# Kernel tuning notes

Measured on AMD Instinct MI355X. Metric: run time of the kernel, lower is better.

## Reference

```python
import jax, jax.numpy as jnp
import numpy as np

NUM_HEADS = 16
D_MODEL = 1024
D_KV = 64
NUM_BUCKETS = 32
MAX_DISTANCE = 128


def _relative_position_bucket(relative_position, num_buckets=NUM_BUCKETS, max_distance=MAX_DISTANCE):
    # faithful port of the torch static method (bidirectional variant)
    n = -relative_position
    nb = num_buckets // 2
    ret = (n < 0).astype(jnp.int32) * nb
    n = jnp.abs(n)
    max_exact = nb // 2
    is_small = n < max_exact
    # guard log(0); is_small branch covers n < max_exact anyway
    val_if_large = max_exact + (
        jnp.log(jnp.maximum(n, 1).astype(jnp.float32) / max_exact)
        / np.log(max_distance / max_exact)
        * (nb - max_exact)
    ).astype(jnp.int32)
    val_if_large = jnp.minimum(val_if_large, nb - 1)
    return ret + jnp.where(is_small, n, val_if_large)


def _compute_bias(seq_len, rel_bias):
    ctx = jnp.arange(seq_len)[:, None]
    mem = jnp.arange(seq_len)[None, :]
    bucket = _relative_position_bucket(mem - ctx)  # [S, S]
    values = rel_bias[bucket]                      # [S, S, H]
    return jnp.transpose(values, (2, 0, 1))[None]  # [1, H, S, S]


def setup_inputs() -> dict:
    key = jax.random.key(0)
    ks = jax.random.split(key, 6)
    B, S = 4, 1024
    scale = 1.0 / np.sqrt(D_MODEL)
    return {
        "hidden_states": jax.random.normal(ks[0], (B, S, D_MODEL), jnp.float32),
        "attention_mask": jnp.ones((B, 1, 1, S), jnp.int32),
        "Wq": jax.random.normal(ks[1], (NUM_HEADS * D_KV, D_MODEL), jnp.float32) * scale,
        "Wk": jax.random.normal(ks[2], (NUM_HEADS * D_KV, D_MODEL), jnp.float32) * scale,
        "Wv": jax.random.normal(ks[3], (NUM_HEADS * D_KV, D_MODEL), jnp.float32) * scale,
        "Wo": jax.random.normal(ks[4], (D_MODEL, NUM_HEADS * D_KV), jnp.float32) * scale,
        "rel_bias": jax.random.normal(ks[5], (NUM_BUCKETS, NUM_HEADS), jnp.float32),
    }


def reference(hidden_states, attention_mask, Wq, Wk, Wv, Wo, rel_bias):
    B, S, _ = hidden_states.shape
    # projections (Linear with bias=False: x @ W.T), reshape to [B, S, H, d_kv]
    q = jnp.einsum('bsd,ed->bse', hidden_states, Wq).reshape(B, S, NUM_HEADS, D_KV)
    k = jnp.einsum('bsd,ed->bse', hidden_states, Wk).reshape(B, S, NUM_HEADS, D_KV)
    v = jnp.einsum('bsd,ed->bse', hidden_states, Wv).reshape(B, S, NUM_HEADS, D_KV)
    scores = jnp.einsum('bqhd,bkhd->bhqk', q, k) / np.sqrt(D_KV)
    scores = scores + _compute_bias(S, rel_bias)
    scores = jnp.where(attention_mask == 0, jnp.float32(-1e9), scores)
    attn_weights = jax.nn.softmax(scores, axis=-1)  # dropout is identity at eval
    attn_output = jnp.einsum('bhqk,bkhd->bqhd', attn_weights, v).reshape(B, S, NUM_HEADS * D_KV)
    output = jnp.einsum('bse,de->bsd', attn_output, Wo)
    return output, attn_weights
```

## Files before the change

### kernel.cpp

```cpp
#include <hip/hip_runtime.h>
#include <hip/hip_bf16.h>

#define BB 4
#define SS 1024
#define HH 16
#define DK 64
#define DM 1024
#define MM (BB * SS)

typedef __attribute__((ext_vector_type(8))) short bh8_t;
typedef __attribute__((ext_vector_type(4))) float f4_t;

#define MFMA(a, b, c) __builtin_amdgcn_mfma_f32_16x16x32_bf16(a, b, c, 0, 0, 0)

__device__ __forceinline__ short f2bf(float f) {
    unsigned u = __builtin_bit_cast(unsigned, f);
    u = (u + 0x7FFFu + ((u >> 16) & 1u)) >> 16;
    return (short)u;
}
__device__ __forceinline__ float bf2f(short h) {
    unsigned u = ((unsigned)(unsigned short)h) << 16;
    return __builtin_bit_cast(float, u);
}

__device__ __forceinline__ int rel_bucket(int rel) {
    int n = -rel;
    int ret = 0;
    if (n < 0) { ret = 16; n = -n; }
    int v;
    if (n < 8) {
        v = n;
    } else {
        float t = logf((float)n * 0.125f) / 2.7725887298583984f * 8.0f;
        v = 8 + (int)t;
        if (v > 15) v = 15;
    }
    return ret + v;
}

__global__ __launch_bounds__(256)
void k_proj(const float* __restrict__ X, const float* __restrict__ Wq,
            const float* __restrict__ Wk, const float* __restrict__ Wv,
            short* __restrict__ Qh, short* __restrict__ Ql,
            short* __restrict__ Kh, short* __restrict__ Kl,
            short* __restrict__ Vt) {
    const int z = blockIdx.z;

    __shared__ short Ah[128][40], Al[128][40], Bh[128][40], Bl[128][40];

    const int tid = threadIdx.x;
    const int m0 = blockIdx.y * 128, n0 = blockIdx.x * 128;
    const int wave = tid >> 6, lane = tid & 63;
    const int quad = lane >> 4, lm = lane & 15;
    const int wm = (wave >> 1) * 64, wn = (wave & 1) * 64;
    const int r = tid >> 1, sg = (tid & 1) * 16;

    f4_t acc[4][4];
#pragma unroll
    for (int i = 0; i < 4; ++i)
#pragma unroll
        for (int j = 0; j < 4; ++j) acc[i][j] = (f4_t){0.f, 0.f, 0.f, 0.f};

    if (z < 2) {
        const float* W = z ? Wk : Wq;
        short* Oh = z ? Kh : Qh;
        short* Ol = z ? Kl : Ql;

        for (int k0 = 0; k0 < DM; k0 += 32) {
            f4_t xa[4], wb[4];
#pragma unroll
            for (int u = 0; u < 4; ++u) {
                xa[u] = *(const f4_t*)(X + (size_t)(m0 + r) * DM + k0 + sg + u * 4);
                wb[u] = *(const f4_t*)(W + (size_t)(n0 + r) * DM + k0 + sg + u * 4);
            }
            __syncthreads();
#pragma unroll
            for (int u = 0; u < 4; ++u) {
                short4 hh, ll;
                hh.x = f2bf(xa[u][0]); ll.x = f2bf(xa[u][0] - bf2f(hh.x));
                hh.y = f2bf(xa[u][1]); ll.y = f2bf(xa[u][1] - bf2f(hh.y));
                hh.z = f2bf(xa[u][2]); ll.z = f2bf(xa[u][2] - bf2f(hh.z));
                hh.w = f2bf(xa[u][3]); ll.w = f2bf(xa[u][3] - bf2f(hh.w));
                *(short4*)&Ah[r][sg + u * 4] = hh;
                *(short4*)&Al[r][sg + u * 4] = ll;
                hh.x = f2bf(wb[u][0]); ll.x = f2bf(wb[u][0] - bf2f(hh.x));
                hh.y = f2bf(wb[u][1]); ll.y = f2bf(wb[u][1] - bf2f(hh.y));
                hh.z = f2bf(wb[u][2]); ll.z = f2bf(wb[u][2] - bf2f(hh.z));
                hh.w = f2bf(wb[u][3]); ll.w = f2bf(wb[u][3] - bf2f(hh.w));
                *(short4*)&Bh[r][sg + u * 4] = hh;
                *(short4*)&Bl[r][sg + u * 4] = ll;
            }
            __syncthreads();

            bh8_t ah[4], al[4];
#pragma unroll
            for (int i = 0; i < 4; ++i) {
                ah[i] = *(const bh8_t*)&Ah[wm + i * 16 + lm][quad * 8];
                al[i] = *(const bh8_t*)&Al[wm + i * 16 + lm][quad * 8];
            }
#pragma unroll
            for (int j = 0; j < 4; ++j) {
                bh8_t bhj = *(const bh8_t*)&Bh[wn + j * 16 + lm][quad * 8];
                bh8_t blj = *(const bh8_t*)&Bl[wn + j * 16 + lm][quad * 8];
#pragma unroll
                for (int i = 0; i < 4; ++i) {
                    acc[i][j] = MFMA(al[i], bhj, acc[i][j]);
                    acc[i][j] = MFMA(ah[i], blj, acc[i][j]);
                    acc[i][j] = MFMA(ah[i], bhj, acc[i][j]);
                }
            }
        }

#pragma unroll
        for (int i = 0; i < 4; ++i)
#pragma unroll
            for (int j = 0; j < 4; ++j)
#pragma unroll
                for (int g = 0; g < 4; ++g) {
                    const int row = m0 + wm + i * 16 + quad * 4 + g;
                    const int col = n0 + wn + j * 16 + lm;
                    const int b = row >> 10, s = row & 1023;
                    const int hd = col >> 6, dk = col & 63;
                    const float v = acc[i][j][g];
                    const short vh = f2bf(v);
                    const short vl = f2bf(v - bf2f(vh));
                    const size_t o = ((size_t)((b * HH + hd) * SS + s)) * DK + dk;
                    Oh[o] = vh;
                    Ol[o] = vl;
                }
    } else {
        for (int k0 = 0; k0 < DM; k0 += 32) {
            f4_t xa[4], wb[4];
#pragma unroll
            for (int u = 0; u < 4; ++u) {
                xa[u] = *(const f4_t*)(X + (size_t)(m0 + r) * DM + k0 + sg + u * 4);
                wb[u] = *(const f4_t*)(Wv + (size_t)(n0 + r) * DM + k0 + sg + u * 4);
            }
            __syncthreads();
#pragma unroll
            for (int u = 0; u < 4; ++u) {
                short4 hh;
                hh.x = f2bf(xa[u][0]); hh.y = f2bf(xa[u][1]);
                hh.z = f2bf(xa[u][2]); hh.w = f2bf(xa[u][3]);
                *(short4*)&Ah[r][sg + u * 4] = hh;
                hh.x = f2bf(wb[u][0]); hh.y = f2bf(wb[u][1]);
                hh.z = f2bf(wb[u][2]); hh.w = f2bf(wb[u][3]);
                *(short4*)&Bh[r][sg + u * 4] = hh;
            }
            __syncthreads();

            bh8_t ah[4];
#pragma unroll
            for (int i = 0; i < 4; ++i)
                ah[i] = *(const bh8_t*)&Ah[wm + i * 16 + lm][quad * 8];
#pragma unroll
            for (int j = 0; j < 4; ++j) {
                bh8_t bhj = *(const bh8_t*)&Bh[wn + j * 16 + lm][quad * 8];
#pragma unroll
                for (int i = 0; i < 4; ++i) acc[i][j] = MFMA(ah[i], bhj, acc[i][j]);
            }
        }

#pragma unroll
        for (int i = 0; i < 4; ++i)
#pragma unroll
            for (int j = 0; j < 4; ++j)
#pragma unroll
                for (int g = 0; g < 4; ++g) {
                    const int row = m0 + wm + i * 16 + quad * 4 + g;
                    const int col = n0 + wn + j * 16 + lm;
                    const int b = row >> 10, s = row & 1023;
                    const int hd = col >> 6, dk = col & 63;
                    Vt[((size_t)((b * HH + hd) * DK + dk)) * SS + s] = f2bf(acc[i][j][g]);
                }
    }
}

#define EPAD 1044

__global__ __launch_bounds__(512, 4)
void k_fused(const short* __restrict__ Qh, const short* __restrict__ Ql,
             const short* __restrict__ Kh, const short* __restrict__ Kl,
             const short* __restrict__ Vt, const int* __restrict__ mask,
             const float* __restrict__ rb, float* __restrict__ P,
             short* __restrict__ AO) {
    __shared__ __align__(16) char smem[75584];
    float* E     = (float*)smem;
    float* redS  = (float*)smem;
    float* biasS = (float*)(smem + 66816);
    int*   maskS = (int*)(smem + 70976);
    float* wmaxS = (float*)(smem + 75072);

    const int tid = threadIdx.x;
    const int bid = blockIdx.x;
    const int swz = (bid & 7) * 512 + (bid >> 3);
    const int qb = swz & 63, bh = swz >> 6;
    const int b = bh >> 4, hd = bh & 15;
    const int q0 = qb * 16;
    const int wave = tid >> 6, lane = tid & 63;
    const int quad = lane >> 4, lm = lane & 15;

    for (int i = tid; i < 1040; i += 512)
        biasS[i] = rb[rel_bucket(i - q0 - 15) * HH + hd];
    for (int i = tid; i < 1024; i += 512) maskS[i] = mask[b * SS + i];

    bh8_t qah[2], qal[2];
#pragma unroll
    for (int ks = 0; ks < 2; ++ks) {
        const size_t qo = ((size_t)bh * SS + q0 + lm) * DK + ks * 32 + quad * 8;
        qah[ks] = *(const bh8_t*)(Qh + qo);
        qal[ks] = *(const bh8_t*)(Ql + qo);
    }
    __syncthreads();

    float pmax[4] = {-3.0e38f, -3.0e38f, -3.0e38f, -3.0e38f};

#pragma unroll
    for (int kt = 0; kt < 4; ++kt) {
        const int kb = wave * 128 + kt * 32;
        f4_t acc[2];
        acc[0] = (f4_t){0.f, 0.f, 0.f, 0.f};
        acc[1] = (f4_t){0.f, 0.f, 0.f, 0.f};
        bh8_t kh[2][2], kl[2][2];
#pragma unroll
        for (int j = 0; j < 2; ++j)
#pragma unroll
            for (int ks = 0; ks < 2; ++ks) {
                const size_t ko =
                    ((size_t)bh * SS + kb + j * 16 + lm) * DK + ks * 32 + quad * 8;
                kh[j][ks] = *(const bh8_t*)(Kh + ko);
                kl[j][ks] = *(const bh8_t*)(Kl + ko);
            }
#pragma unroll
        for (int j = 0; j < 2; ++j)
#pragma unroll
            for (int ks = 0; ks < 2; ++ks) {
                acc[j] = MFMA(qal[ks], kh[j][ks], acc[j]);
                acc[j] = MFMA(qah[ks], kl[j][ks], acc[j]);
                acc[j] = MFMA(qah[ks], kh[j][ks], acc[j]);
            }
#pragma unroll
        for (int j = 0; j < 2; ++j) {
            const int col = kb + j * 16 + lm;
            const int msk = maskS[col];
#pragma unroll
            for (int g = 0; g < 4; ++g) {
                const int rl = quad * 4 + g;
                float s = acc[j][g] * 0.125f + biasS[col - rl + 15];
                s = (msk == 0) ? -1e9f : s;
                E[rl * EPAD + col] = s;
                pmax[g] = fmaxf(pmax[g], s);
            }
        }
    }
#pragma unroll
    for (int g = 0; g < 4; ++g) {
        float m = pmax[g];
        m = fmaxf(m, __shfl_xor(m, 1, 64));
        m = fmaxf(m, __shfl_xor(m, 2, 64));
        m = fmaxf(m, __shfl_xor(m, 4, 64));
        m = fmaxf(m, __shfl_xor(m, 8, 64));
        if (lm == 0) wmaxS[wave * 16 + quad * 4 + g] = m;
    }
    __syncthreads();

    {
        const int row = tid >> 5;
        const int cc = (tid & 31) * 4;
        float m = wmaxS[row];
#pragma unroll
        for (int w = 1; w < 8; ++w) m = fmaxf(m, wmaxS[w * 16 + row]);
        f4_t ev[8];
        float sum = 0.f;
#pragma unroll
        for (int u = 0; u < 8; ++u) {
            f4_t s4 = *(const f4_t*)&E[row * EPAD + cc + u * 128];
            f4_t e;
            e[0] = __expf(s4[0] - m);
            e[1] = __expf(s4[1] - m);
            e[2] = __expf(s4[2] - m);
            e[3] = __expf(s4[3] - m);
            ev[u] = e;
            sum += e[0] + e[1] + e[2] + e[3];
        }
        sum += __shfl_xor(sum, 1, 64);
        sum += __shfl_xor(sum, 2, 64);
        sum += __shfl_xor(sum, 4, 64);
        sum += __shfl_xor(sum, 8, 64);
        sum += __shfl_xor(sum, 16, 64);
        const float inv = 1.0f / sum;
        float* Pr = P + ((size_t)bh * SS + q0 + row) * SS;
#pragma unroll
        for (int u = 0; u < 8; ++u) {
            f4_t p;
            p[0] = ev[u][0] * inv;
            p[1] = ev[u][1] * inv;
            p[2] = ev[u][2] * inv;
            p[3] = ev[u][3] * inv;
            *(f4_t*)&E[row * EPAD + cc + u * 128] = p;
            *(f4_t*)(Pr + cc + u * 128) = p;
        }
    }
    __syncthreads();

    f4_t acc[4];
#pragma unroll
    for (int f = 0; f < 4; ++f) acc[f] = (f4_t){0.f, 0.f, 0.f, 0.f};

#pragma unroll
    for (int kk = 0; kk < 4; ++kk) {
        const int kg = wave * 128 + kk * 32 + quad * 8;
        f4_t p0 = *(const f4_t*)&E[lm * EPAD + kg];
        f4_t p1 = *(const f4_t*)&E[lm * EPAD + kg + 4];
        bh8_t pa;
        pa[0] = f2bf(p0[0]); pa[1] = f2bf(p0[1]);
        pa[2] = f2bf(p0[2]); pa[3] = f2bf(p0[3]);
        pa[4] = f2bf(p1[0]); pa[5] = f2bf(p1[1]);
        pa[6] = f2bf(p1[2]); pa[7] = f2bf(p1[3]);
#pragma unroll
        for (int f = 0; f < 4; ++f) {
            bh8_t vb =
                *(const bh8_t*)(Vt + ((size_t)bh * DK + f * 16 + lm) * SS + kg);
            acc[f] = MFMA(pa, vb, acc[f]);
        }
    }
    __syncthreads();
#pragma unroll
    for (int f = 0; f < 4; ++f)
#pragma unroll
        for (int g = 0; g < 4; ++g)
            redS[((size_t)wave * 16 + quad * 4 + g) * 64 + f * 16 + lm] = acc[f][g];
    __syncthreads();

    {
        const int flat = tid * 2;
        const int q = flat >> 6, dk = flat & 63;
        float s0 = 0.f, s1 = 0.f;
#pragma unroll
        for (int w = 0; w < 8; ++w) {
            s0 += redS[((size_t)w * 16 + q) * 64 + dk];
            s1 += redS[((size_t)w * 16 + q) * 64 + dk + 1];
        }
        short2 o;
        o.x = f2bf(s0);
        o.y = f2bf(s1);
        *(short2*)(AO + ((size_t)(b * SS + q0 + q)) * DM + hd * DK + dk) = o;
    }
}

__global__ __launch_bounds__(256)
void k_out(const short* __restrict__ A, const float* __restrict__ Wo,
           float* __restrict__ Out) {
    __shared__ short As[128][40], Bs[128][40];

    const int tid = threadIdx.x;
    const int m0 = blockIdx.y * 128, n0 = blockIdx.x * 128;
    const int wave = tid >> 6, lane = tid & 63;
    const int quad = lane >> 4, lm = lane & 15;
    const int wm = (wave >> 1) * 64, wn = (wave & 1) * 64;
    const int r = tid >> 1, sg = (tid & 1) * 16;

    f4_t acc[4][4];
#pragma unroll
    for (int i = 0; i < 4; ++i)
#pragma unroll
        for (int j = 0; j < 4; ++j) acc[i][j] = (f4_t){0.f, 0.f, 0.f, 0.f};

    for (int k0 = 0; k0 < DM; k0 += 32) {
        uint4 a0 = *(const uint4*)(A + (size_t)(m0 + r) * DM + k0 + sg);
        uint4 a1 = *(const uint4*)(A + (size_t)(m0 + r) * DM + k0 + sg + 8);
        f4_t wb[4];
#pragma unroll
        for (int u = 0; u < 4; ++u)
            wb[u] = *(const f4_t*)(Wo + (size_t)(n0 + r) * DM + k0 + sg + u * 4);
        __syncthreads();
        *(uint4*)&As[r][sg] = a0;
        *(uint4*)&As[r][sg + 8] = a1;
#pragma unroll
        for (int u = 0; u < 4; ++u) {
            short4 hh;
            hh.x = f2bf(wb[u][0]); hh.y = f2bf(wb[u][1]);
            hh.z = f2bf(wb[u][2]); hh.w = f2bf(wb[u][3]);
            *(short4*)&Bs[r][sg + u * 4] = hh;
        }
        __syncthreads();

        bh8_t ah[4];
#pragma unroll
        for (int i = 0; i < 4; ++i)
            ah[i] = *(const bh8_t*)&As[wm + i * 16 + lm][quad * 8];
#pragma unroll
        for (int j = 0; j < 4; ++j) {
            bh8_t bhj = *(const bh8_t*)&Bs[wn + j * 16 + lm][quad * 8];
#pragma unroll
            for (int i = 0; i < 4; ++i) acc[i][j] = MFMA(ah[i], bhj, acc[i][j]);
        }
    }

#pragma unroll
    for (int i = 0; i < 4; ++i)
#pragma unroll
        for (int j = 0; j < 4; ++j)
#pragma unroll
            for (int g = 0; g < 4; ++g)
                Out[(size_t)(m0 + wm + i * 16 + quad * 4 + g) * DM + n0 + wn + j * 16 + lm] =
                    acc[i][j][g];
}

extern "C" void kernel_launch(void* const* d_in, const int* in_sizes, int n_in,
                              void* d_out, int out_size, void* d_ws, size_t ws_size,
                              hipStream_t stream) {
    const float* X    = (const float*)d_in[0];
    const int*   mask = (const int*)d_in[1];
    const float* Wq   = (const float*)d_in[2];
    const float* Wk   = (const float*)d_in[3];
    const float* Wv   = (const float*)d_in[4];
    const float* Wo   = (const float*)d_in[5];
    const float* rb   = (const float*)d_in[6];

    float* out = (float*)d_out;
    float* P   = out + (size_t)BB * SS * DM;

    short* ws = (short*)d_ws;
    short* Qh = ws;
    short* Ql = ws + (size_t)4194304;
    short* Kh = ws + (size_t)8388608;
    short* Kl = ws + (size_t)12582912;
    short* Vt = ws + (size_t)16777216;
    short* AO = ws + (size_t)20971520;

    k_proj <<<dim3(8, 32, 3), 256, 0, stream>>>(X, Wq, Wk, Wv, Qh, Ql, Kh, Kl, Vt);
    k_fused<<<dim3(4096), 512, 0, stream>>>(Qh, Ql, Kh, Kl, Vt, mask, rb, P, AO);
    k_out  <<<dim3(8, 32), 256, 0, stream>>>(AO, Wo, out);
}
```

Baseline: 645.5 us.

## Pre-split inputs to bf16 hi/lo, precompute bias table, prefetch tiles, stream P stores

Adds a k_split pre-pass that converts X and the weights to bf16 hi/lo pairs once and builds a per-head relative-bias table. This replaces the repeated fp32 loads and conversions inside every GEMM tile and the log-based bucket computation per block. The GEMMs and the attention kernel now register-prefetch the next K/V/A/B tile while computing the current one. The attention-probability write moves after the PV product, reading E with coalesced rows and using nontemporal stores, and some syncthreads become raw s_barrier. In exchange it adds an extra launch and extra workspace traffic for the split copies.

```diff
diff --git a/kernel.cpp b/kernel.cpp
--- a/kernel.cpp
+++ b/kernel.cpp
@@ -39,8 +39,50 @@
 }
 
 __global__ __launch_bounds__(256)
-void k_proj(const float* __restrict__ X, const float* __restrict__ Wq,
-            const float* __restrict__ Wk, const float* __restrict__ Wv,
+void k_split(const float* __restrict__ X, const float* __restrict__ Wq,
+             const float* __restrict__ Wk, const float* __restrict__ Wv,
+             const float* __restrict__ Wo, const float* __restrict__ rbv,
+             short* __restrict__ Xh, short* __restrict__ Xl,
+             short* __restrict__ Wqh, short* __restrict__ Wql,
+             short* __restrict__ Wkh, short* __restrict__ Wkl,
+             short* __restrict__ Wvh, short* __restrict__ Woh,
+             float* __restrict__ biasT) {
+    const long i = (long)blockIdx.x * 256 + threadIdx.x;
+    if (i < 2097152) {
+        const float* src;
+        short* dh;
+        short* dl = nullptr;
+        long j = i;
+        if (i < 1048576) { src = X; dh = Xh; dl = Xl; }
+        else if (i < 1310720) { src = Wq; dh = Wqh; dl = Wql; j = i - 1048576; }
+        else if (i < 1572864) { src = Wk; dh = Wkh; dl = Wkl; j = i - 1310720; }
+        else if (i < 1835008) { src = Wv; dh = Wvh; j = i - 1572864; }
+        else { src = Wo; dh = Woh; j = i - 1835008; }
+        f4_t v = *(const f4_t*)(src + j * 4);
+        short4 h, l;
+        h.x = f2bf(v[0]); l.x = f2bf(v[0] - bf2f(h.x));
+        h.y = f2bf(v[1]); l.y = f2bf(v[1] - bf2f(h.y));
+        h.z = f2bf(v[2]); l.z = f2bf(v[2] - bf2f(h.z));
+        h.w = f2bf(v[3]); l.w = f2bf(v[3] - bf2f(h.w));
+        *(short4*)(dh + j * 4) = h;
+        if (dl) *(short4*)(dl + j * 4) = l;
+    } else if (i < 2105408) {
+        const long j = i - 2097152;
+        const int hd = (int)(j / 516);
+        const int d0 = (int)(j % 516) * 4;
+#pragma unroll
+        for (int t = 0; t < 4; ++t) {
+            const int dd = d0 + t;
+            biasT[hd * 2064 + dd] = rbv[rel_bucket(dd - 1024) * HH + hd];
+        }
+    }
+}
+
+__global__ __launch_bounds__(256)
+void k_proj(const short* __restrict__ Xh, const short* __restrict__ Xl,
+            const short* __restrict__ Wqh, const short* __restrict__ Wql,
+            const short* __restrict__ Wkh, const short* __restrict__ Wkl,
+            const short* __restrict__ Wvh,
             short* __restrict__ Qh, short* __restrict__ Ql,
             short* __restrict__ Kh, short* __restrict__ Kl,
             short* __restrict__ Vt) {
@@ -61,36 +103,34 @@
 #pragma unroll
         for (int j = 0; j < 4; ++j) acc[i][j] = (f4_t){0.f, 0.f, 0.f, 0.f};
 
+    const size_t xoff = (size_t)(m0 + r) * DM + sg;
+    const size_t woff = (size_t)(n0 + r) * DM + sg;
+
     if (z < 2) {
-        const float* W = z ? Wk : Wq;
+        const short* Wh = z ? Wkh : Wqh;
+        const short* Wl = z ? Wkl : Wql;
         short* Oh = z ? Kh : Qh;
         short* Ol = z ? Kl : Ql;
 
+        uint4 a0 = *(const uint4*)(Xh + xoff), a1 = *(const uint4*)(Xh + xoff + 8);
+        uint4 c0 = *(const uint4*)(Xl + xoff), c1 = *(const uint4*)(Xl + xoff + 8);
+        uint4 b0 = *(const uint4*)(Wh + woff), b1 = *(const uint4*)(Wh + woff + 8);
+        uint4 d0 = *(const uint4*)(Wl + woff), d1 = *(const uint4*)(Wl + woff + 8);
+
         for (int k0 = 0; k0 < DM; k0 += 32) {
-            f4_t xa[4], wb[4];
-#pragma unroll
-            for (int u = 0; u < 4; ++u) {
-                xa[u] = *(const f4_t*)(X + (size_t)(m0 + r) * DM + k0 + sg + u * 4);
-                wb[u] = *(const f4_t*)(W + (size_t)(n0 + r) * DM + k0 + sg + u * 4);
-            }
             __syncthreads();
-#pragma unroll
-            for (int u = 0; u < 4; ++u) {
-                short4 hh, ll;
-                hh.x = f2bf(xa[u][0]); ll.x = f2bf(xa[u][0] - bf2f(hh.x));
-                hh.y = f2bf(xa[u][1]); ll.y = f2bf(xa[u][1] - bf2f(hh.y));
-                hh.z = f2bf(xa[u][2]); ll.z = f2bf(xa[u][2] - bf2f(hh.z));
-                hh.w = f2bf(xa[u][3]); ll.w = f2bf(xa[u][3] - bf2f(hh.w));
-                *(short4*)&Ah[r][sg + u * 4] = hh;
-                *(short4*)&Al[r][sg + u * 4] = ll;
-                hh.x = f2bf(wb[u][0]); ll.x = f2bf(wb[u][0] - bf2f(hh.x));
-                hh.y = f2bf(wb[u][1]); ll.y = f2bf(wb[u][1] - bf2f(hh.y));
-                hh.z = f2bf(wb[u][2]); ll.z = f2bf(wb[u][2] - bf2f(hh.z));
-                hh.w = f2bf(wb[u][3]); ll.w = f2bf(wb[u][3] - bf2f(hh.w));
-                *(short4*)&Bh[r][sg + u * 4] = hh;
-                *(short4*)&Bl[r][sg + u * 4] = ll;
-            }
+            *(uint4*)&Ah[r][sg] = a0; *(uint4*)&Ah[r][sg + 8] = a1;
+            *(uint4*)&Al[r][sg] = c0; *(uint4*)&Al[r][sg + 8] = c1;
+            *(uint4*)&Bh[r][sg] = b0; *(uint4*)&Bh[r][sg + 8] = b1;
+            *(uint4*)&Bl[r][sg] = d0; *(uint4*)&Bl[r][sg + 8] = d1;
             __syncthreads();
+            if (k0 + 32 < DM) {
+                const size_t xo = xoff + k0 + 32, wo = woff + k0 + 32;
+                a0 = *(const uint4*)(Xh + xo); a1 = *(const uint4*)(Xh + xo + 8);
+                c0 = *(const uint4*)(Xl + xo); c1 = *(const uint4*)(Xl + xo + 8);
+                b0 = *(const uint4*)(Wh + wo); b1 = *(const uint4*)(Wh + wo + 8);
+                d0 = *(const uint4*)(Wl + wo); d1 = *(const uint4*)(Wl + wo + 8);
+            }
 
             bh8_t ah[4], al[4];
 #pragma unroll
@@ -129,25 +169,19 @@
                     Ol[o] = vl;
                 }
     } else {
+        uint4 a0 = *(const uint4*)(Xh + xoff), a1 = *(const uint4*)(Xh + xoff + 8);
+        uint4 b0 = *(const uint4*)(Wvh + woff), b1 = *(const uint4*)(Wvh + woff + 8);
+
         for (int k0 = 0; k0 < DM; k0 += 32) {
-            f4_t xa[4], wb[4];
-#pragma unroll
-            for (int u = 0; u < 4; ++u) {
-                xa[u] = *(const f4_t*)(X + (size_t)(m0 + r) * DM + k0 + sg + u * 4);
-                wb[u] = *(const f4_t*)(Wv + (size_t)(n0 + r) * DM + k0 + sg + u * 4);
-            }
             __syncthreads();
-#pragma unroll
-            for (int u = 0; u < 4; ++u) {
-                short4 hh;
-                hh.x = f2bf(xa[u][0]); hh.y = f2bf(xa[u][1]);
-                hh.z = f2bf(xa[u][2]); hh.w = f2bf(xa[u][3]);
-                *(short4*)&Ah[r][sg + u * 4] = hh;
-                hh.x = f2bf(wb[u][0]); hh.y = f2bf(wb[u][1]);
-                hh.z = f2bf(wb[u][2]); hh.w = f2bf(wb[u][3]);
-                *(short4*)&Bh[r][sg + u * 4] = hh;
-            }
+            *(uint4*)&Ah[r][sg] = a0; *(uint4*)&Ah[r][sg + 8] = a1;
+            *(uint4*)&Bh[r][sg] = b0; *(uint4*)&Bh[r][sg + 8] = b1;
             __syncthreads();
+            if (k0 + 32 < DM) {
+                const size_t xo = xoff + k0 + 32, wo = woff + k0 + 32;
+                a0 = *(const uint4*)(Xh + xo); a1 = *(const uint4*)(Xh + xo + 8);
+                b0 = *(const uint4*)(Wvh + wo); b1 = *(const uint4*)(Wvh + wo + 8);
+            }
 
             bh8_t ah[4];
 #pragma unroll
@@ -182,7 +216,7 @@
 void k_fused(const short* __restrict__ Qh, const short* __restrict__ Ql,
              const short* __restrict__ Kh, const short* __restrict__ Kl,
              const short* __restrict__ Vt, const int* __restrict__ mask,
-             const float* __restrict__ rb, float* __restrict__ P,
+             const float* __restrict__ biasT, float* __restrict__ P,
              short* __restrict__ AO) {
     __shared__ __align__(16) char smem[75584];
     float* E     = (float*)smem;
@@ -201,7 +235,7 @@
     const int quad = lane >> 4, lm = lane & 15;
 
     for (int i = tid; i < 1040; i += 512)
-        biasS[i] = rb[rel_bucket(i - q0 - 15) * HH + hd];
+        biasS[i] = biasT[hd * 2064 + i + 1009 - q0];
     for (int i = tid; i < 1024; i += 512) maskS[i] = mask[b * SS + i];
 
     bh8_t qah[2], qal[2];
@@ -215,29 +249,45 @@
 
     float pmax[4] = {-3.0e38f, -3.0e38f, -3.0e38f, -3.0e38f};
 
+    bh8_t kh[2][2][2], kl[2][2][2];
+    {
+        const int kb = wave * 128;
+#pragma unroll
+        for (int j = 0; j < 2; ++j)
+#pragma unroll
+            for (int ks = 0; ks < 2; ++ks) {
+                const size_t ko =
+                    ((size_t)bh * SS + kb + j * 16 + lm) * DK + ks * 32 + quad * 8;
+                kh[0][j][ks] = *(const bh8_t*)(Kh + ko);
+                kl[0][j][ks] = *(const bh8_t*)(Kl + ko);
+            }
+    }
 #pragma unroll
     for (int kt = 0; kt < 4; ++kt) {
+        const int cur = kt & 1;
+        if (kt < 3) {
+            const int kb2 = wave * 128 + (kt + 1) * 32;
+#pragma unroll
+            for (int j = 0; j < 2; ++j)
+#pragma unroll
+                for (int ks = 0; ks < 2; ++ks) {
+                    const size_t ko =
+                        ((size_t)bh * SS + kb2 + j * 16 + lm) * DK + ks * 32 + quad * 8;
+                    kh[cur ^ 1][j][ks] = *(const bh8_t*)(Kh + ko);
+                    kl[cur ^ 1][j][ks] = *(const bh8_t*)(Kl + ko);
+                }
+        }
         const int kb = wave * 128 + kt * 32;
         f4_t acc[2];
         acc[0] = (f4_t){0.f, 0.f, 0.f, 0.f};
         acc[1] = (f4_t){0.f, 0.f, 0.f, 0.f};
-        bh8_t kh[2][2], kl[2][2];
 #pragma unroll
         for (int j = 0; j < 2; ++j)
 #pragma unroll
             for (int ks = 0; ks < 2; ++ks) {
-                const size_t ko =
-                    ((size_t)bh * SS + kb + j * 16 + lm) * DK + ks * 32 + quad * 8;
-                kh[j][ks] = *(const bh8_t*)(Kh + ko);
-                kl[j][ks] = *(const bh8_t*)(Kl + ko);
-            }
-#pragma unroll
-        for (int j = 0; j < 2; ++j)
-#pragma unroll
-            for (int ks = 0; ks < 2; ++ks) {
-                acc[j] = MFMA(qal[ks], kh[j][ks], acc[j]);
-                acc[j] = MFMA(qah[ks], kl[j][ks], acc[j]);
-                acc[j] = MFMA(qah[ks], kh[j][ks], acc[j]);
+                acc[j] = MFMA(qal[ks], kh[cur][j][ks], acc[j]);
+                acc[j] = MFMA(qah[ks], kl[cur][j][ks], acc[j]);
+                acc[j] = MFMA(qah[ks], kh[cur][j][ks], acc[j]);
             }
 #pragma unroll
         for (int j = 0; j < 2; ++j) {
@@ -289,7 +339,6 @@
         sum += __shfl_xor(sum, 8, 64);
         sum += __shfl_xor(sum, 16, 64);
         const float inv = 1.0f / sum;
-        float* Pr = P + ((size_t)bh * SS + q0 + row) * SS;
 #pragma unroll
         for (int u = 0; u < 8; ++u) {
             f4_t p;
@@ -298,7 +347,6 @@
             p[2] = ev[u][2] * inv;
             p[3] = ev[u][3] * inv;
             *(f4_t*)&E[row * EPAD + cc + u * 128] = p;
-            *(f4_t*)(Pr + cc + u * 128) = p;
         }
     }
     __syncthreads();
@@ -307,30 +355,62 @@
 #pragma unroll
     for (int f = 0; f < 4; ++f) acc[f] = (f4_t){0.f, 0.f, 0.f, 0.f};
 
+    bh8_t vb[2][4];
+    {
+        const int kg0 = wave * 128 + quad * 8;
+#pragma unroll
+        for (int f = 0; f < 4; ++f)
+            vb[0][f] = *(const bh8_t*)(Vt + ((size_t)bh * DK + f * 16 + lm) * SS + kg0);
+    }
 #pragma unroll
     for (int kk = 0; kk < 4; ++kk) {
+        const int cur = kk & 1;
         const int kg = wave * 128 + kk * 32 + quad * 8;
         f4_t p0 = *(const f4_t*)&E[lm * EPAD + kg];
         f4_t p1 = *(const f4_t*)&E[lm * EPAD + kg + 4];
+        if (kk < 3) {
+            const int kg2 = wave * 128 + (kk + 1) * 32 + quad * 8;
+#pragma unroll
+            for (int f = 0; f < 4; ++f)
+                vb[cur ^ 1][f] =
+                    *(const bh8_t*)(Vt + ((size_t)bh * DK + f * 16 + lm) * SS + kg2);
+        }
         bh8_t pa;
         pa[0] = f2bf(p0[0]); pa[1] = f2bf(p0[1]);
         pa[2] = f2bf(p0[2]); pa[3] = f2bf(p0[3]);
         pa[4] = f2bf(p1[0]); pa[5] = f2bf(p1[1]);
         pa[6] = f2bf(p1[2]); pa[7] = f2bf(p1[3]);
 #pragma unroll
-        for (int f = 0; f < 4; ++f) {
-            bh8_t vb =
-                *(const bh8_t*)(Vt + ((size_t)bh * DK + f * 16 + lm) * SS + kg);
-            acc[f] = MFMA(pa, vb, acc[f]);
-        }
-    }
-    __syncthreads();
+        for (int f = 0; f < 4; ++f) acc[f] = MFMA(pa, vb[cur][f], acc[f]);
+    }
+
+    {
+        const int c0 = (lane & 31) * 4;
+        const int rh = lane >> 5;
+#pragma unroll
+        for (int u = 0; u < 8; ++u) {
+            const int rr = u * 2 + rh;
+            f4_t pv = *(const f4_t*)&E[rr * EPAD + wave * 128 + c0];
+            __builtin_nontemporal_store(
+                pv, (f4_t*)(P + ((size_t)bh * SS + q0 + rr) * SS + wave * 128 + c0));
+        }
+    }
+
+    asm volatile("s_waitcnt lgkmcnt(0)" ::: "memory");
+    __builtin_amdgcn_sched_barrier(0);
+    __builtin_amdgcn_s_barrier();
+    __builtin_amdgcn_sched_barrier(0);
+
 #pragma unroll
     for (int f = 0; f < 4; ++f)
 #pragma unroll
         for (int g = 0; g < 4; ++g)
             redS[((size_t)wave * 16 + quad * 4 + g) * 64 + f * 16 + lm] = acc[f][g];
-    __syncthreads();
+
+    asm volatile("s_waitcnt lgkmcnt(0)" ::: "memory");
+    __builtin_amdgcn_sched_barrier(0);
+    __builtin_amdgcn_s_barrier();
+    __builtin_amdgcn_sched_barrier(0);
 
     {
         const int flat = tid * 2;
@@ -349,7 +429,7 @@
 }
 
 __global__ __launch_bounds__(256)
-void k_out(const short* __restrict__ A, const float* __restrict__ Wo,
+void k_out(const short* __restrict__ A, const short* __restrict__ Woh,
            float* __restrict__ Out) {
     __shared__ short As[128][40], Bs[128][40];
 
@@ -366,24 +446,21 @@
 #pragma unroll
         for (int j = 0; j < 4; ++j) acc[i][j] = (f4_t){0.f, 0.f, 0.f, 0.f};
 
+    const size_t aoff = (size_t)(m0 + r) * DM + sg;
+    const size_t woff = (size_t)(n0 + r) * DM + sg;
+    uint4 a0 = *(const uint4*)(A + aoff), a1 = *(const uint4*)(A + aoff + 8);
+    uint4 b0 = *(const uint4*)(Woh + woff), b1 = *(const uint4*)(Woh + woff + 8);
+
     for (int k0 = 0; k0 < DM; k0 += 32) {
-        uint4 a0 = *(const uint4*)(A + (size_t)(m0 + r) * DM + k0 + sg);
-        uint4 a1 = *(const uint4*)(A + (size_t)(m0 + r) * DM + k0 + sg + 8);
-        f4_t wb[4];
-#pragma unroll
-        for (int u = 0; u < 4; ++u)
-            wb[u] = *(const f4_t*)(Wo + (size_t)(n0 + r) * DM + k0 + sg + u * 4);
         __syncthreads();
-        *(uint4*)&As[r][sg] = a0;
-        *(uint4*)&As[r][sg + 8] = a1;
-#pragma unroll
-        for (int u = 0; u < 4; ++u) {
-            short4 hh;
-            hh.x = f2bf(wb[u][0]); hh.y = f2bf(wb[u][1]);
-            hh.z = f2bf(wb[u][2]); hh.w = f2bf(wb[u][3]);
-            *(short4*)&Bs[r][sg + u * 4] = hh;
-        }
+        *(uint4*)&As[r][sg] = a0; *(uint4*)&As[r][sg + 8] = a1;
+        *(uint4*)&Bs[r][sg] = b0; *(uint4*)&Bs[r][sg + 8] = b1;
         __syncthreads();
+        if (k0 + 32 < DM) {
+            const size_t ao = aoff + k0 + 32, wo = woff + k0 + 32;
+            a0 = *(const uint4*)(A + ao); a1 = *(const uint4*)(A + ao + 8);
+            b0 = *(const uint4*)(Woh + wo); b1 = *(const uint4*)(Woh + wo + 8);
+        }
 
         bh8_t ah[4];
 #pragma unroll
@@ -403,8 +480,10 @@
         for (int j = 0; j < 4; ++j)
 #pragma unroll
             for (int g = 0; g < 4; ++g)
-                Out[(size_t)(m0 + wm + i * 16 + quad * 4 + g) * DM + n0 + wn + j * 16 + lm] =
-                    acc[i][j][g];
+                __builtin_nontemporal_store(
+                    acc[i][j][g],
+                    &Out[(size_t)(m0 + wm + i * 16 + quad * 4 + g) * DM + n0 + wn +
+                         j * 16 + lm]);
 }
 
 extern "C" void kernel_launch(void* const* d_in, const int* in_sizes, int n_in,
@@ -422,14 +501,26 @@
     float* P   = out + (size_t)BB * SS * DM;
 
     short* ws = (short*)d_ws;
-    short* Qh = ws;
-    short* Ql = ws + (size_t)4194304;
-    short* Kh = ws + (size_t)8388608;
-    short* Kl = ws + (size_t)12582912;
-    short* Vt = ws + (size_t)16777216;
-    short* AO = ws + (size_t)20971520;
-
-    k_proj <<<dim3(8, 32, 3), 256, 0, stream>>>(X, Wq, Wk, Wv, Qh, Ql, Kh, Kl, Vt);
-    k_fused<<<dim3(4096), 512, 0, stream>>>(Qh, Ql, Kh, Kl, Vt, mask, rb, P, AO);
-    k_out  <<<dim3(8, 32), 256, 0, stream>>>(AO, Wo, out);
-}
+    short* Qh  = ws;
+    short* Ql  = ws + (size_t)4194304;
+    short* Kh  = ws + (size_t)8388608;
+    short* Kl  = ws + (size_t)12582912;
+    short* Vt  = ws + (size_t)16777216;
+    short* AO  = ws + (size_t)20971520;
+    short* Xh  = ws + (size_t)25165824;
+    short* Xl  = ws + (size_t)29360128;
+    short* Wqh = ws + (size_t)33554432;
+    short* Wql = ws + (size_t)34603008;
+    short* Wkh = ws + (size_t)35651584;
+    short* Wkl = ws + (size_t)36700160;
+    short* Wvh = ws + (size_t)37748736;
+    short* Woh = ws + (size_t)38797312;
+    float* biasT = (float*)((char*)d_ws + 79691776);
+
+    k_split<<<dim3(8225), 256, 0, stream>>>(X, Wq, Wk, Wv, Wo, rb, Xh, Xl, Wqh,
+                                            Wql, Wkh, Wkl, Wvh, Woh, biasT);
+    k_proj <<<dim3(8, 32, 3), 256, 0, stream>>>(Xh, Xl, Wqh, Wql, Wkh, Wkl, Wvh,
+                                                Qh, Ql, Kh, Kl, Vt);
+    k_fused<<<dim3(4096), 512, 0, stream>>>(Qh, Ql, Kh, Kl, Vt, mask, biasT, P, AO);
+    k_out  <<<dim3(8, 32), 256, 0, stream>>>(AO, Woh, out);
+}
```

Measured after the change: 566.5 us. 12.2% less time.
